# Optimization experiments

Hardware: AMD Instinct MI355X
Metric: run time of the kernel (lower is better)

Reference implementation:

```python
import jax, jax.numpy as jnp
import numpy as np

UP = 512      # up_size
RADIUS = 60   # revise crop radius -> 120x120 squares
COEF = 1.5    # COM threshold coefficient
DOT = 4       # intensity-adjust circle radius
B = 16
M = 4
BASE = 128


def _affine_grid(theta, H, W):
    # torch F.affine_grid, align_corners=False. theta: (2,3) -> grid (H,W,2) with (x,y)
    xs = (2.0 * jnp.arange(W, dtype=jnp.float32) + 1.0) / W - 1.0
    ys = (2.0 * jnp.arange(H, dtype=jnp.float32) + 1.0) / H - 1.0
    X, Y = jnp.meshgrid(xs, ys)  # (H,W), X varies along width
    base = jnp.stack([X, Y, jnp.ones_like(X)], axis=-1)  # (H,W,3)
    return base @ theta.T  # (H,W,2)


def _gs_one(im, gr):
    # torch F.grid_sample, bilinear, zero padding, align_corners=False
    # im: (C,H,W), gr: (Hg,Wg,2) -> (C,Hg,Wg)
    C, H, W = im.shape
    x = ((gr[..., 0] + 1.0) * W - 1.0) * 0.5
    y = ((gr[..., 1] + 1.0) * H - 1.0) * 0.5
    x0 = jnp.floor(x)
    y0 = jnp.floor(y)
    wx = x - x0
    wy = y - y0

    def tap(ix, iy, w):
        valid = (ix >= 0) & (ix < W) & (iy >= 0) & (iy < H)
        ii = jnp.clip(iy, 0, H - 1).astype(jnp.int32)
        jj = jnp.clip(ix, 0, W - 1).astype(jnp.int32)
        return im[:, ii, jj] * (jnp.where(valid, w, 0.0))[None]

    return (tap(x0, y0, (1 - wx) * (1 - wy))
            + tap(x0 + 1, y0, wx * (1 - wy))
            + tap(x0, y0 + 1, (1 - wx) * wy)
            + tap(x0 + 1, y0 + 1, wx * wy))


_grid_sample = jax.vmap(_gs_one)  # (B,C,H,W),(B,Hg,Wg,2)->(B,C,Hg,Wg)


def _inv2x3(theta):
    # append [0,0,1], invert 3x3, keep top 2 rows (as in Joint.forward)
    n = theta.shape[0]
    bottom = jnp.broadcast_to(jnp.array([[0.0, 0.0, 1.0]], jnp.float32), (n, 1, 3))
    full = jnp.concatenate([theta, bottom], axis=1)
    return jnp.linalg.inv(full)[:, :2]


def _com(img, mask, coef):
    # center_of_mass: threshold = coef * mean over mask, intensity-weighted centroid
    H, W = img.shape
    msum = jnp.maximum(mask.sum(), 1.0)
    thr = (img.sum() / msum) * coef
    w = jnp.where(img > thr, img, 0.0)
    tot = w.sum() + 1e-8
    cx = (w.sum(axis=1) * jnp.arange(H, dtype=img.dtype)).sum() / tot  # row
    cy = (w.sum(axis=0) * jnp.arange(W, dtype=img.dtype)).sum() / tot  # col
    return cx, cy


def _revise(image, masks_rot, inv_theta, adj, radius, coef, dot):
    # revise_size_on_affine_gpu with adj_para given and pare_reverse=True
    d = 2 * radius
    yy, xx = jnp.meshgrid(jnp.arange(d), jnp.arange(d), indexing='ij')
    small_sq = ((yy - radius) ** 2 + (xx - radius) ** 2) <= dot ** 2  # dot mask

    def per_item(img_i, new_i, mask_i, th_i, a_i):
        cx, cy = _com(new_i, mask_i, coef)
        x0 = jnp.round(cx).astype(jnp.int32) - radius
        y0 = jnp.round(cy).astype(jnp.int32) - radius
        small = jax.lax.dynamic_slice(img_i[0], (x0, y0), (d, d))
        small = jnp.where(small_sq, small / a_i, small)  # pare_reverse=True -> divide
        out = _gs_one(small[None], _affine_grid(th_i, d, d))  # (1,d,d)
        return jax.lax.dynamic_update_slice(img_i, out, (0, x0, y0))

    img = image
    for j in range(masks_rot.shape[0]):
        mj = masks_rot[j]                 # (B,H,W) float 0/1
        new = image[:, 0] * mj            # COM always from original image*mask
        img = jax.vmap(per_item)(img, new, mj, inv_theta, adj)
    return img


def setup_inputs() -> dict:
    key = jax.random.key(0)
    ks = jax.random.split(key, 6)
    predicted_base = jax.random.uniform(ks[0], (B, 1, BASE, BASE), jnp.float32)
    e = 0.05 * jax.random.normal(ks[1], (B, 4), jnp.float32)
    sc = (jnp.zeros((B, 2, 3), jnp.float32)
          .at[:, 0, 0].set(1.0 + e[:, 0]).at[:, 0, 1].set(e[:, 1])
          .at[:, 1, 0].set(e[:, 2]).at[:, 1, 1].set(1.0 + e[:, 3]))
    ang = jax.random.uniform(ks[2], (B,), jnp.float32, -0.2, 0.2)
    rot = (jnp.zeros((B, 2, 3), jnp.float32)
           .at[:, 0, 0].set(jnp.cos(ang)).at[:, 0, 1].set(-jnp.sin(ang))
           .at[:, 1, 0].set(jnp.sin(ang)).at[:, 1, 1].set(jnp.cos(ang)))
    t = jax.random.uniform(ks[3], (B, 2), jnp.float32, -0.05, 0.05)
    tr = (jnp.zeros((B, 2, 3), jnp.float32)
          .at[:, 0, 0].set(1.0).at[:, 1, 1].set(1.0)
          .at[:, 0, 2].set(t[:, 0]).at[:, 1, 2].set(t[:, 1]))
    adj = jax.random.uniform(ks[4], (B,), jnp.float32, 0.9, 1.1)
    centers = [(128, 128), (128, 384), (384, 128), (384, 384)]
    yy, xx = np.meshgrid(np.arange(UP), np.arange(UP), indexing='ij')
    masks = np.stack([((yy - cy) ** 2 + (xx - cx) ** 2 <= 30 ** 2).astype(np.float32)
                      for (cy, cx) in centers])
    return dict(predicted_base=predicted_base, scaler_shear=sc, rotation=rot,
                translation=tr, adj_mask=adj, masks=jnp.asarray(masks))


def reference(predicted_base, scaler_shear, rotation, translation, adj_mask, masks):
    b = predicted_base.shape[0]
    it1 = _inv2x3(scaler_shear)
    it2 = _inv2x3(rotation)
    it3 = _inv2x3(translation)
    base_inp = jax.image.resize(predicted_base, (b, 1, UP, UP), method='linear')
    mk_grid = jax.vmap(lambda th: _affine_grid(th, UP, UP))
    g1, g2, g3 = mk_grid(it1), mk_grid(it2), mk_grid(it3)
    pred_trans = _grid_sample(base_inp, g3)
    pred_rot = _grid_sample(pred_trans, g2)
    pred_input = _grid_sample(pred_rot, g1)
    # rotate masks through grid_2 then grid_1, threshold at 0.5
    new_masks = []
    for j in range(masks.shape[0]):
        bm = jnp.broadcast_to(masks[j][None, None], (b, 1, UP, UP))
        rm = _grid_sample(_grid_sample(bm, g2), g1)
        new_masks.append(rm[:, 0] >= 0.5)
    masks_rot = jnp.stack(new_masks)  # (M,B,UP,UP) bool
    pred_revise = _revise(pred_input, masks_rot.astype(pred_input.dtype), it1,
                          adj_mask, RADIUS, COEF, DOT)
    return (base_inp, pred_input, pred_revise, masks_rot)
```

## Files before the change

### kernel.cpp

```cpp
#include <hip/hip_runtime.h>
#include <math.h>
#include <limits.h>

#define NPIX (512*512)
#define NB 16
#define RAD 60
#define DSZ 120
#define PSTR 121
#define GTS 48
#define GSTR 49


__device__ __forceinline__ float gs_bilinear(const float* img, int H, int W,
                                             float gx, float gy) {
    float x = ((gx + 1.0f) * (float)W - 1.0f) * 0.5f;
    float y = ((gy + 1.0f) * (float)H - 1.0f) * 0.5f;
    float xf = floorf(x), yf = floorf(y);
    int ix = (int)xf, iy = (int)yf;
    float wx = x - xf, wy = y - yf;
    float v = 0.0f;
    bool vx0 = (ix >= 0) && (ix < W);
    bool vx1 = (ix >= -1) && (ix < W - 1);
    bool vy0 = (iy >= 0) && (iy < H);
    bool vy1 = (iy >= -1) && (iy < H - 1);
    if (vx0 && vy0) v += img[iy*W + ix]         * ((1.0f - wx) * (1.0f - wy));
    if (vx1 && vy0) v += img[iy*W + ix + 1]     * (wx * (1.0f - wy));
    if (vx0 && vy1) v += img[(iy+1)*W + ix]     * ((1.0f - wx) * wy);
    if (vx1 && vy1) v += img[(iy+1)*W + ix + 1] * (wx * wy);
    return v;
}

__device__ __forceinline__ float gs_bilinear_patch(const float* img, float gx, float gy) {
    float x = ((gx + 1.0f) * 120.0f - 1.0f) * 0.5f;
    float y = ((gy + 1.0f) * 120.0f - 1.0f) * 0.5f;
    float xf = floorf(x), yf = floorf(y);
    int ix = (int)xf, iy = (int)yf;
    float wx = x - xf, wy = y - yf;
    float v = 0.0f;
    bool vx0 = (ix >= 0) && (ix < 120);
    bool vx1 = (ix >= -1) && (ix < 119);
    bool vy0 = (iy >= 0) && (iy < 120);
    bool vy1 = (iy >= -1) && (iy < 119);
    if (vx0 && vy0) v += img[iy*PSTR + ix]         * ((1.0f - wx) * (1.0f - wy));
    if (vx1 && vy0) v += img[iy*PSTR + ix + 1]     * (wx * (1.0f - wy));
    if (vx0 && vy1) v += img[(iy+1)*PSTR + ix]     * ((1.0f - wx) * wy);
    if (vx1 && vy1) v += img[(iy+1)*PSTR + ix + 1] * (wx * wy);
    return v;
}

__global__ void __launch_bounds__(256) k_init(const float* __restrict__ base,
                                              const float* __restrict__ sc,
                                              const float* __restrict__ rot,
                                              const float* __restrict__ tr,
                                              const float* __restrict__ masks,
                                              float* __restrict__ out0,
                                              float* __restrict__ ws_inv,
                                              int* __restrict__ bbox,
                                              unsigned* __restrict__ occ,
                                              int* __restrict__ qcount) {
    int bid = blockIdx.x;
    if (bid < 4096) {
        int b = bid >> 8;
        int p4 = (bid & 255) * 256 + threadIdx.x;
        int p = p4 * 4;
        int y = p >> 9, x0p = p & 511;
        const float* src = base + b * 128 * 128;
        float r[4];
        float sy = (float)y * 0.25f - 0.375f;
        float fy0 = floorf(sy);
        int iy = (int)fy0;
        float fy = sy - fy0;
        int iy0 = min(max(iy, 0), 127), iy1 = min(max(iy + 1, 0), 127);
        #pragma unroll
        for (int k = 0; k < 4; ++k) {
            int x = x0p + k;
            float sx = (float)x * 0.25f - 0.375f;
            float fx0 = floorf(sx);
            int ix = (int)fx0;
            float fx = sx - fx0;
            int ix0 = min(max(ix, 0), 127), ix1 = min(max(ix + 1, 0), 127);
            float v00 = src[iy0 * 128 + ix0], v10 = src[iy0 * 128 + ix1];
            float v01 = src[iy1 * 128 + ix0], v11 = src[iy1 * 128 + ix1];
            r[k] = (v00 * (1.0f - fx) + v10 * fx) * (1.0f - fy)
                 + (v01 * (1.0f - fx) + v11 * fx) * fy;
        }
        *(float4*)(out0 + (size_t)b * NPIX + p) = make_float4(r[0], r[1], r[2], r[3]);
    } else if (bid < 4128) {
        int word = (bid - 4096) * 4 + (threadIdx.x >> 6);
        int lane = threadIdx.x & 63;
        int j = word >> 5, ty = word & 31;
        const float* mk = masks + (size_t)j * NPIX + ty * 16 * 512 + lane * 8;
        int any = 0;
        for (int rr = 0; rr < 16; ++rr) {
            const float4* p = (const float4*)(mk + rr * 512);
            float4 a = p[0], c = p[1];
            if (a.x != 0.f || a.y != 0.f || a.z != 0.f || a.w != 0.f ||
                c.x != 0.f || c.y != 0.f || c.z != 0.f || c.w != 0.f) any = 1;
        }
        unsigned long long bb = __ballot(any);
        if (lane == 0) {
            unsigned wrd = 0;
            for (int tx = 0; tx < 32; ++tx)
                if (bb & (3ull << (2 * tx))) wrd |= 1u << tx;
            occ[j * 32 + ty] = wrd;
        }
    } else {
        int t = threadIdx.x;
        if (t < 48) {
            int m = t >> 4, b = t & 15;
            const float* th = (m == 0 ? sc : (m == 1 ? rot : tr)) + b * 6;
            float a  = th[0], bbv = th[1], tx = th[2];
            float c  = th[3], d   = th[4], ty = th[5];
            float L10 = c / a;
            float dp  = d  - L10 * bbv;
            float typ = ty - L10 * tx;
            float i10 = (0.0f - L10) / dp;
            float i00 = (1.0f - bbv * i10) / a;
            float i11 = 1.0f / dp;
            float i01 = (0.0f - bbv * i11) / a;
            float i12 = (0.0f - typ) / dp;
            float i02 = (0.0f - bbv * i12 - tx) / a;
            float* o = ws_inv + m * 96 + b * 6;
            o[0] = i00; o[1] = i01; o[2] = i02;
            o[3] = i10; o[4] = i11; o[5] = i12;
        }
        bbox[t] = ((t & 3) < 2) ? INT_MAX : INT_MIN;
        if (t == 0) *qcount = 0;
    }
}

__device__ __forceinline__ void gsample_tile(const float* __restrict__ src,
                                             float* __restrict__ dst,
                                             float* __restrict__ dst2,
                                             const float* __restrict__ thetas,
                                             int b, int tile, float* tb) {
    int ox = (tile & 15) * 32, oy = (tile >> 4) * 32;
    const float* th = thetas + b * 6;
    float t0 = th[0], t1 = th[1], t2 = th[2], t3 = th[3], t4 = th[4], t5 = th[5];
    const float* im = src + (size_t)b * NPIX;

    float sxmin = 1e30f, sxmax = -1e30f, symin = 1e30f, symax = -1e30f;
    #pragma unroll
    for (int cy = 0; cy < 2; ++cy)
        #pragma unroll
        for (int cx = 0; cx < 2; ++cx) {
            float X = (2.0f * (float)(ox + cx * 31) + 1.0f) / 512.0f - 1.0f;
            float Y = (2.0f * (float)(oy + cy * 31) + 1.0f) / 512.0f - 1.0f;
            float gx = t0 * X + t1 * Y + t2;
            float gy = t3 * X + t4 * Y + t5;
            float sx = ((gx + 1.0f) * 512.0f - 1.0f) * 0.5f;
            float sy = ((gy + 1.0f) * 512.0f - 1.0f) * 0.5f;
            sxmin = fminf(sxmin, sx); sxmax = fmaxf(sxmax, sx);
            symin = fminf(symin, sy); symax = fmaxf(symax, sy);
        }
    int rx0 = (int)floorf(sxmin) - 1;
    int ry0 = (int)floorf(symin) - 1;
    bool fits = ((int)floorf(sxmax) + 2 - rx0 < GTS) &&
                ((int)floorf(symax) + 2 - ry0 < GTS);

    int t = threadIdx.x;
    int py = oy + (t >> 3);
    int px0 = ox + (t & 7) * 4;
    float Y = (2.0f * (float)py + 1.0f) / 512.0f - 1.0f;
    float r[4];

    if (fits) {
        for (int i = t; i < GTS * GTS; i += 256) {
            int rr = i / GTS, cc = i - rr * GTS;
            int gy_ = ry0 + rr, gx_ = rx0 + cc;
            float v = 0.0f;
            if (gx_ >= 0 && gx_ < 512 && gy_ >= 0 && gy_ < 512)
                v = im[gy_ * 512 + gx_];
            tb[rr * GSTR + cc] = v;
        }
        __syncthreads();
        #pragma unroll
        for (int k = 0; k < 4; ++k) {
            float X = (2.0f * (float)(px0 + k) + 1.0f) / 512.0f - 1.0f;
            float gx = t0 * X + t1 * Y + t2;
            float gy = t3 * X + t4 * Y + t5;
            float x = ((gx + 1.0f) * 512.0f - 1.0f) * 0.5f;
            float y = ((gy + 1.0f) * 512.0f - 1.0f) * 0.5f;
            float xf = floorf(x), yf = floorf(y);
            int ix = (int)xf, iy = (int)yf;
            float wx = x - xf, wy = y - yf;
            int lx = ix - rx0, ly = iy - ry0;
            float v;
            v  = tb[ly * GSTR + lx]           * ((1.0f - wx) * (1.0f - wy));
            v += tb[ly * GSTR + lx + 1]       * (wx * (1.0f - wy));
            v += tb[(ly + 1) * GSTR + lx]     * ((1.0f - wx) * wy);
            v += tb[(ly + 1) * GSTR + lx + 1] * (wx * wy);
            r[k] = v;
        }
    } else {
        #pragma unroll
        for (int k = 0; k < 4; ++k) {
            float X = (2.0f * (float)(px0 + k) + 1.0f) / 512.0f - 1.0f;
            float gx = t0 * X + t1 * Y + t2;
            float gy = t3 * X + t4 * Y + t5;
            r[k] = gs_bilinear(im, 512, 512, gx, gy);
        }
    }
    float4 v4 = make_float4(r[0], r[1], r[2], r[3]);
    size_t op = (size_t)b * NPIX + py * 512 + px0;
    *(float4*)(dst + op) = v4;
    if (dst2) *(float4*)(dst2 + op) = v4;
}

__global__ void __launch_bounds__(256) k_g3ot(const float* __restrict__ src,
                                              float* __restrict__ dst,
                                              const float* __restrict__ inv3,
                                              const unsigned* __restrict__ occ,
                                              const float* __restrict__ inv1,
                                              const float* __restrict__ inv2,
                                              unsigned char* __restrict__ otile,
                                              int* __restrict__ queue,
                                              int* __restrict__ qcount) {
    __shared__ float tb[GTS * GSTR];
    int bid = blockIdx.x;
    if (bid < 4096) {
        gsample_tile(src, dst, nullptr, inv3, bid >> 8, bid & 255, tb);
        return;
    }
    int idx = (bid - 4096) * 256 + threadIdx.x;
    int jb = idx >> 10, tile = idx & 1023;
    int j = jb >> 4, b = jb & 15;
    int ty = tile >> 5, tx = tile & 31;
    const float* t1 = inv1 + b * 6;
    const float* t2 = inv2 + b * 6;
    float xs[2] = { (float)(tx * 16), (float)(tx * 16 + 15) };
    float ys[2] = { (float)(ty * 16), (float)(ty * 16 + 15) };
    float sxmin = 1e30f, sxmax = -1e30f, symin = 1e30f, symax = -1e30f;
    for (int cy = 0; cy < 2; ++cy)
        for (int cx = 0; cx < 2; ++cx) {
            float X = (2.0f * xs[cx] + 1.0f) / 512.0f - 1.0f;
            float Y = (2.0f * ys[cy] + 1.0f) / 512.0f - 1.0f;
            float gx = t1[0] * X + t1[1] * Y + t1[2];
            float gy = t1[3] * X + t1[4] * Y + t1[5];
            float sx = ((gx + 1.0f) * 512.0f - 1.0f) * 0.5f;
            float sy = ((gy + 1.0f) * 512.0f - 1.0f) * 0.5f;
            sxmin = fminf(sxmin, sx); sxmax = fmaxf(sxmax, sx);
            symin = fminf(symin, sy); symax = fmaxf(symax, sy);
        }
    int c0 = max((int)floorf(sxmin) - 1, 0), c1 = min((int)floorf(sxmax) + 2, 511);
    int r0 = max((int)floorf(symin) - 1, 0), r1 = min((int)floorf(symax) + 2, 511);
    bool any = false;
    if (c0 <= c1 && r0 <= r1) {
        float A0 = t2[0], A1 = t2[1], A3 = t2[3], A4 = t2[4];
        float Kx = 0.5f * (-511.0f * (A0 + A1) + 512.0f * t2[2] + 511.0f);
        float Ky = 0.5f * (-511.0f * (A3 + A4) + 512.0f * t2[5] + 511.0f);
        float pxmin = A0 * (A0 >= 0.f ? c0 : c1) + A1 * (A1 >= 0.f ? r0 : r1) + Kx;
        float pxmax = A0 * (A0 >= 0.f ? c1 : c0) + A1 * (A1 >= 0.f ? r1 : r0) + Kx;
        float pymin = A3 * (A3 >= 0.f ? c0 : c1) + A4 * (A4 >= 0.f ? r0 : r1) + Ky;
        float pymax = A3 * (A3 >= 0.f ? c1 : c0) + A4 * (A4 >= 0.f ? r1 : r0) + Ky;
        int xlo = max((int)floorf(pxmin) - 1, 0), xhi = min((int)floorf(pxmax) + 2, 511);
        int ylo = max((int)floorf(pymin) - 1, 0), yhi = min((int)floorf(pymax) + 2, 511);
        if (xlo <= xhi && ylo <= yhi)
            for (int tr = ylo >> 4; tr <= yhi >> 4; ++tr)
                for (int tc = xlo >> 4; tc <= xhi >> 4; ++tc)
                    if ((occ[j * 32 + tr] >> tc) & 1u) any = true;
    }
    otile[idx] = any ? 1 : 0;
    if (any) {
        int pos = atomicAdd(qcount, 1);
        queue[pos] = (jb << 10) | tile;
    }
}

__global__ void __launch_bounds__(256) k_gsample(const float* __restrict__ src,
                                                 float* __restrict__ dst,
                                                 float* __restrict__ dst2,
                                                 const float* __restrict__ thetas) {
    __shared__ float tb[GTS * GSTR];
    gsample_tile(src, dst, dst2, thetas, blockIdx.x >> 8, blockIdx.x & 255, tb);
}

__device__ __forceinline__ float rm2_val(const float* mk, const float* t2, int cx_, int ry_) {
    float X2 = (2.0f * (float)cx_ + 1.0f) / 512.0f - 1.0f;
    float Y2 = (2.0f * (float)ry_ + 1.0f) / 512.0f - 1.0f;
    float g2x = t2[0] * X2 + t2[1] * Y2 + t2[2];
    float g2y = t2[3] * X2 + t2[4] * Y2 + t2[5];
    return gs_bilinear(mk, 512, 512, g2x, g2y);
}

__global__ void __launch_bounds__(256) k_zml(const float* __restrict__ masks,
                                             float* __restrict__ out3,
                                             const float* __restrict__ inv1,
                                             const float* __restrict__ inv2,
                                             const unsigned char* __restrict__ otile,
                                             const int* __restrict__ queue,
                                             const int* __restrict__ qcount,
                                             int* __restrict__ bbox) {
    int bid = blockIdx.x;
    if (bid < 2048) {
        const float4 z4 = make_float4(0.f, 0.f, 0.f, 0.f);
        float4* p = (float4*)out3;
        int stride = 2048 * 256;
        for (int i = bid * 256 + threadIdx.x; i < 64 * NPIX / 4; i += stride) {
            int jb = i >> 16;
            int w = i & 65535;
            int y = w >> 7;
            int x = (w << 2) & 511;
            int tile = ((y >> 4) << 5) | (x >> 4);
            if (!otile[(jb << 10) | tile]) p[i] = z4;
        }
        return;
    }
    __shared__ int sbb[4];
    int n = *qcount;
    for (int q = bid - 2048; q < n; q += 1024) {
        int e = queue[q];
        int jb = e >> 10, tile = e & 1023;
        if (threadIdx.x == 0) { sbb[0] = INT_MAX; sbb[1] = INT_MAX; sbb[2] = INT_MIN; sbb[3] = INT_MIN; }
        __syncthreads();

        int ty = tile >> 5, tx = tile & 31;
        int y = ty * 16 + (threadIdx.x >> 4);
        int x = tx * 16 + (threadIdx.x & 15);
        int j = jb >> 4, b = jb & 15;
        const float* t1 = inv1 + b * 6;
        const float* t2 = inv2 + b * 6;
        const float* mk = masks + (size_t)j * NPIX;

        float X = (2.0f * (float)x + 1.0f) / 512.0f - 1.0f;
        float Y = (2.0f * (float)y + 1.0f) / 512.0f - 1.0f;
        float gx = t1[0] * X + t1[1] * Y + t1[2];
        float gy = t1[3] * X + t1[4] * Y + t1[5];
        float sx = ((gx + 1.0f) * 512.0f - 1.0f) * 0.5f;
        float sy = ((gy + 1.0f) * 512.0f - 1.0f) * 0.5f;
        float xf = floorf(sx), yf = floorf(sy);
        int ix = (int)xf, iy = (int)yf;
        float wx = sx - xf, wy = sy - yf;

        float v = 0.0f;
        bool vx0 = (ix >= 0) && (ix < 512);
        bool vx1 = (ix >= -1) && (ix < 511);
        bool vy0 = (iy >= 0) && (iy < 512);
        bool vy1 = (iy >= -1) && (iy < 511);
        if (vx0 && vy0) v += rm2_val(mk, t2, ix,     iy    ) * ((1.0f - wx) * (1.0f - wy));
        if (vx1 && vy0) v += rm2_val(mk, t2, ix + 1, iy    ) * (wx * (1.0f - wy));
        if (vx0 && vy1) v += rm2_val(mk, t2, ix,     iy + 1) * ((1.0f - wx) * wy);
        if (vx1 && vy1) v += rm2_val(mk, t2, ix + 1, iy + 1) * (wx * wy);

        float res = 0.0f;
        if (v >= 0.5f) {
            res = 1.0f;
            atomicMin(&sbb[0], y); atomicMin(&sbb[1], x);
            atomicMax(&sbb[2], y); atomicMax(&sbb[3], x);
        }
        out3[(size_t)jb * NPIX + y * 512 + x] = res;

        __syncthreads();
        if (threadIdx.x == 0 && sbb[2] != INT_MIN) {
            atomicMin(&bbox[jb * 4 + 0], sbb[0]);
            atomicMin(&bbox[jb * 4 + 1], sbb[1]);
            atomicMax(&bbox[jb * 4 + 2], sbb[2]);
            atomicMax(&bbox[jb * 4 + 3], sbb[3]);
        }
        __syncthreads();
    }
}

__global__ void __launch_bounds__(256) k_stats(const float* __restrict__ pred,
                                               const float* __restrict__ mrot,
                                               const int* __restrict__ bbox,
                                               int* __restrict__ xy) {
    int jb = blockIdx.x;
    int b = jb & 15;
    int rmin = bbox[jb*4+0], cmin = bbox[jb*4+1], rmax = bbox[jb*4+2], cmax = bbox[jb*4+3];
    const float* img = pred + (size_t)b * NPIX;
    const float* mk  = mrot + (size_t)jb * NPIX;
    int lane = threadIdx.x & 63, w = threadIdx.x >> 6;
    int W = cmax - cmin + 1;
    int total = (rmax >= rmin) ? W * (rmax - rmin + 1) : 0;

    double msum = 0.0, isum = 0.0;
    for (int i = threadIdx.x; i < total; i += 256) {
        int r = rmin + i / W, c = cmin + i % W;
        float m = mk[r * 512 + c];
        if (m != 0.0f) {
            msum += (double)m;
            isum += (double)(img[r * 512 + c] * m);
        }
    }
    for (int o = 32; o > 0; o >>= 1) {
        msum += __shfl_down(msum, o, 64);
        isum += __shfl_down(isum, o, 64);
    }
    __shared__ double s0[4], s1[4], s2[4];
    __shared__ double sthr;
    if (lane == 0) { s0[w] = msum; s1[w] = isum; }
    __syncthreads();
    if (threadIdx.x == 0) {
        double M = s0[0] + s0[1] + s0[2] + s0[3];
        double I = s1[0] + s1[1] + s1[2] + s1[3];
        sthr = (I / fmax(M, 1.0)) * 1.5;
    }
    __syncthreads();
    double t = sthr;

    double wsum = 0.0, sy = 0.0, sx = 0.0;
    for (int i = threadIdx.x; i < total; i += 256) {
        int r = rmin + i / W, c = cmin + i % W;
        float m = mk[r * 512 + c];
        if (m != 0.0f) {
            float v = img[r * 512 + c] * m;
            if ((double)v > t) {
                double vd = (double)v;
                wsum += vd;
                sy += vd * (double)r;
                sx += vd * (double)c;
            }
        }
    }
    for (int o = 32; o > 0; o >>= 1) {
        wsum += __shfl_down(wsum, o, 64);
        sy   += __shfl_down(sy,   o, 64);
        sx   += __shfl_down(sx,   o, 64);
    }
    __syncthreads();
    if (lane == 0) { s0[w] = wsum; s1[w] = sy; s2[w] = sx; }
    __syncthreads();
    if (threadIdx.x == 0) {
        double W_ = s0[0] + s0[1] + s0[2] + s0[3];
        double SY = s1[0] + s1[1] + s1[2] + s1[3];
        double SX = s2[0] + s2[1] + s2[2] + s2[3];
        double tot = W_ + 1e-8;
        int x0 = (int)rint(SY / tot) - RAD;
        int y0 = (int)rint(SX / tot) - RAD;
        x0 = min(max(x0, 0), 512 - DSZ);
        y0 = min(max(y0, 0), 512 - DSZ);
        xy[jb * 2 + 0] = x0;
        xy[jb * 2 + 1] = y0;
    }
}

__device__ __forceinline__ void patch_one(float* __restrict__ im, float* __restrict__ patch,
                                          int x0, int y0, float a,
                                          float t0, float t1, float t2,
                                          float t3, float t4, float t5) {
    for (int t = threadIdx.x; t < DSZ * DSZ; t += 1024) {
        int u = t / DSZ, v = t % DSZ;
        float val = im[(x0 + u) * 512 + (y0 + v)];
        int du = u - RAD, dv = v - RAD;
        if (du * du + dv * dv <= 16) val = val / a;
        patch[u * PSTR + v] = val;
    }
    __syncthreads();
    for (int t = threadIdx.x; t < DSZ * DSZ; t += 1024) {
        int py = t / DSZ, px = t % DSZ;
        float X = (2.0f * (float)px + 1.0f) / 120.0f - 1.0f;
        float Y = (2.0f * (float)py + 1.0f) / 120.0f - 1.0f;
        float gx = t0 * X + t1 * Y + t2;
        float gy = t3 * X + t4 * Y + t5;
        float o = gs_bilinear_patch(patch, gx, gy);
        im[(x0 + py) * 512 + (y0 + px)] = o;
    }
}

__global__ void __launch_bounds__(1024) k_patch(float* __restrict__ img,
                                                const int* __restrict__ xy,
                                                const float* __restrict__ inv1,
                                                const float* __restrict__ adj) {
    __shared__ float patch[DSZ * PSTR];
    int b = blockIdx.x >> 2, j = blockIdx.x & 3;
    int rx[4], ry[4];
    #pragma unroll
    for (int k = 0; k < 4; ++k) {
        rx[k] = xy[(k * 16 + b) * 2 + 0];
        ry[k] = xy[(k * 16 + b) * 2 + 1];
    }
    bool overlap = false;
    #pragma unroll
    for (int i = 0; i < 4; ++i)
        #pragma unroll
        for (int k = 0; k < 4; ++k)
            if (i < k && abs(rx[i] - rx[k]) < DSZ && abs(ry[i] - ry[k]) < DSZ)
                overlap = true;

    float a = adj[b];
    float* im = img + (size_t)b * NPIX;
    const float* th = inv1 + b * 6;
    float t0 = th[0], t1 = th[1], t2 = th[2], t3 = th[3], t4 = th[4], t5 = th[5];

    if (!overlap) {
        patch_one(im, patch, rx[j], ry[j], a, t0, t1, t2, t3, t4, t5);
    } else {
        if (j != 0) return;
        for (int jj = 0; jj < 4; ++jj) {
            patch_one(im, patch, rx[jj], ry[jj], a, t0, t1, t2, t3, t4, t5);
            __threadfence_block();
            __syncthreads();
        }
    }
}


extern "C" void kernel_launch(void* const* d_in, const int* in_sizes, int n_in,
                              void* d_out, int out_size, void* d_ws, size_t ws_size,
                              hipStream_t stream) {
    const float* base  = (const float*)d_in[0];
    const float* sc    = (const float*)d_in[1];
    const float* rot   = (const float*)d_in[2];
    const float* tr    = (const float*)d_in[3];
    const float* adj   = (const float*)d_in[4];
    const float* masks = (const float*)d_in[5];

    float* out  = (float*)d_out;
    float* out0 = out;
    float* out1 = out0 + (size_t)NB * NPIX;
    float* out2 = out1 + (size_t)NB * NPIX;
    float* out3 = out2 + (size_t)NB * NPIX;

    float*         inv1   = (float*)d_ws;
    float*         inv2   = inv1 + 96;
    float*         inv3   = inv1 + 192;
    int*           xy     = (int*)((char*)d_ws + 4096);
    int*           bbox   = (int*)((char*)d_ws + 8192);
    unsigned*      occ    = (unsigned*)((char*)d_ws + 12288);
    int*           qcount = (int*)((char*)d_ws + 16128);
    unsigned char* otile  = (unsigned char*)((char*)d_ws + 16384);
    int*           queue  = (int*)((char*)d_ws + 81920);

    k_init<<<4129, 256, 0, stream>>>(base, sc, rot, tr, masks, out0,
                                     (float*)d_ws, bbox, occ, qcount);
    k_g3ot<<<4352, 256, 0, stream>>>(out0, out2, inv3, occ, inv1, inv2,
                                     otile, queue, qcount);
    k_gsample<<<4096, 256, 0, stream>>>(out2, out3, nullptr, inv2);
    k_gsample<<<4096, 256, 0, stream>>>(out3, out1, out2, inv1);
    k_zml<<<3072, 256, 0, stream>>>(masks, out3, inv1, inv2, otile, queue, qcount, bbox);
    k_stats<<<64, 256, 0, stream>>>(out1, out3, bbox, xy);
    k_patch<<<64, 1024, 0, stream>>>(out2, xy, inv1, adj);
}
```

Measured before the change: 248.6 us.

## Fuse upsample and three chained grid samples into one tiled kernel

Replaces the upsample pass and the three separate grid-sample kernels with one kernel. Per output tile it works back through the inverse affine chain to find the source regions, recomputes the upsampled base into shared memory, and applies the translate, rotate and scale samples stage by stage in LDS. This drops the full-resolution intermediate writes and reads between stages and two kernel launches. In exchange each block uses more shared memory and redundantly recomputes halo regions, and tiles whose footprint does not fit fall back to a very expensive nested per-pixel evaluation.

Result: no change. 248.4 us (-0.1%).

```diff
diff --git a/kernel.cpp b/kernel.cpp
--- a/kernel.cpp
+++ b/kernel.cpp
@@ -7,8 +7,13 @@
 #define RAD 60
 #define DSZ 120
 #define PSTR 121
-#define GTS 48
-#define GSTR 49
+
+#define C1 48
+#define SR_S 49
+#define C2 62
+#define ST_S 63
+#define C3 66
+#define SB_S 67
 
 
 __device__ __forceinline__ float gs_bilinear(const float* img, int H, int W,
@@ -48,45 +53,91 @@
     return v;
 }
 
-__global__ void __launch_bounds__(256) k_init(const float* __restrict__ base,
-                                              const float* __restrict__ sc,
-                                              const float* __restrict__ rot,
-                                              const float* __restrict__ tr,
-                                              const float* __restrict__ masks,
-                                              float* __restrict__ out0,
-                                              float* __restrict__ ws_inv,
-                                              int* __restrict__ bbox,
-                                              unsigned* __restrict__ occ,
-                                              int* __restrict__ qcount) {
+__device__ __forceinline__ float upsample_val(const float* __restrict__ src, int y, int x) {
+    float sy = (float)y * 0.25f - 0.375f;
+    float fy0 = floorf(sy);
+    int iy = (int)fy0;
+    float fy = sy - fy0;
+    int iy0 = min(max(iy, 0), 127), iy1 = min(max(iy + 1, 0), 127);
+    float sx = (float)x * 0.25f - 0.375f;
+    float fx0 = floorf(sx);
+    int ix = (int)fx0;
+    float fx = sx - fx0;
+    int ix0 = min(max(ix, 0), 127), ix1 = min(max(ix + 1, 0), 127);
+    float v00 = src[iy0 * 128 + ix0], v10 = src[iy0 * 128 + ix1];
+    float v01 = src[iy1 * 128 + ix0], v11 = src[iy1 * 128 + ix1];
+    return (v00 * (1.0f - fx) + v10 * fx) * (1.0f - fy)
+         + (v01 * (1.0f - fx) + v11 * fx) * fy;
+}
+
+__device__ __forceinline__ void smap512(const float* th, float x, float y,
+                                        float& sx, float& sy) {
+    float X = (2.0f * x + 1.0f) / 512.0f - 1.0f;
+    float Y = (2.0f * y + 1.0f) / 512.0f - 1.0f;
+    float gx = th[0] * X + th[1] * Y + th[2];
+    float gy = th[3] * X + th[4] * Y + th[5];
+    sx = ((gx + 1.0f) * 512.0f - 1.0f) * 0.5f;
+    sy = ((gy + 1.0f) * 512.0f - 1.0f) * 0.5f;
+}
+
+__device__ __forceinline__ void corner_bbox(const float* th, float x0, float x1,
+                                            float y0, float y1,
+                                            int& lx, int& ly, int& w, int& h) {
+    float sxmin = 1e30f, sxmax = -1e30f, symin = 1e30f, symax = -1e30f;
+    #pragma unroll
+    for (int cy = 0; cy < 2; ++cy)
+        #pragma unroll
+        for (int cx = 0; cx < 2; ++cx) {
+            float sx, sy;
+            smap512(th, cx ? x1 : x0, cy ? y1 : y0, sx, sy);
+            sxmin = fminf(sxmin, sx); sxmax = fmaxf(sxmax, sx);
+            symin = fminf(symin, sy); symax = fmaxf(symax, sy);
+        }
+    lx = (int)floorf(sxmin) - 1;
+    ly = (int)floorf(symin) - 1;
+    w  = (int)floorf(sxmax) + 2 - lx + 1;
+    h  = (int)floorf(symax) + 2 - ly + 1;
+}
+
+__device__ __forceinline__ float fb_binp(const float* bs, int x, int y) {
+    if (x < 0 || x >= 512 || y < 0 || y >= 512) return 0.0f;
+    return upsample_val(bs, y, x);
+}
+__device__ __forceinline__ float fb_trans(const float* bs, const float* th3, int x, int y) {
+    if (x < 0 || x >= 512 || y < 0 || y >= 512) return 0.0f;
+    float sx, sy; smap512(th3, (float)x, (float)y, sx, sy);
+    float xf = floorf(sx), yf = floorf(sy);
+    int ix = (int)xf, iy = (int)yf;
+    float wx = sx - xf, wy = sy - yf;
+    return fb_binp(bs, ix, iy)         * ((1.0f - wx) * (1.0f - wy))
+         + fb_binp(bs, ix + 1, iy)     * (wx * (1.0f - wy))
+         + fb_binp(bs, ix, iy + 1)     * ((1.0f - wx) * wy)
+         + fb_binp(bs, ix + 1, iy + 1) * (wx * wy);
+}
+__device__ __forceinline__ float fb_rot(const float* bs, const float* th2,
+                                        const float* th3, int x, int y) {
+    if (x < 0 || x >= 512 || y < 0 || y >= 512) return 0.0f;
+    float sx, sy; smap512(th2, (float)x, (float)y, sx, sy);
+    float xf = floorf(sx), yf = floorf(sy);
+    int ix = (int)xf, iy = (int)yf;
+    float wx = sx - xf, wy = sy - yf;
+    return fb_trans(bs, th3, ix, iy)         * ((1.0f - wx) * (1.0f - wy))
+         + fb_trans(bs, th3, ix + 1, iy)     * (wx * (1.0f - wy))
+         + fb_trans(bs, th3, ix, iy + 1)     * ((1.0f - wx) * wy)
+         + fb_trans(bs, th3, ix + 1, iy + 1) * (wx * wy);
+}
+
+__global__ void __launch_bounds__(256) k_pre(const float* __restrict__ sc,
+                                             const float* __restrict__ rot,
+                                             const float* __restrict__ tr,
+                                             const float* __restrict__ masks,
+                                             float* __restrict__ ws_inv,
+                                             int* __restrict__ bbox,
+                                             unsigned* __restrict__ occ,
+                                             int* __restrict__ qcount) {
     int bid = blockIdx.x;
-    if (bid < 4096) {
-        int b = bid >> 8;
-        int p4 = (bid & 255) * 256 + threadIdx.x;
-        int p = p4 * 4;
-        int y = p >> 9, x0p = p & 511;
-        const float* src = base + b * 128 * 128;
-        float r[4];
-        float sy = (float)y * 0.25f - 0.375f;
-        float fy0 = floorf(sy);
-        int iy = (int)fy0;
-        float fy = sy - fy0;
-        int iy0 = min(max(iy, 0), 127), iy1 = min(max(iy + 1, 0), 127);
-        #pragma unroll
-        for (int k = 0; k < 4; ++k) {
-            int x = x0p + k;
-            float sx = (float)x * 0.25f - 0.375f;
-            float fx0 = floorf(sx);
-            int ix = (int)fx0;
-            float fx = sx - fx0;
-            int ix0 = min(max(ix, 0), 127), ix1 = min(max(ix + 1, 0), 127);
-            float v00 = src[iy0 * 128 + ix0], v10 = src[iy0 * 128 + ix1];
-            float v01 = src[iy1 * 128 + ix0], v11 = src[iy1 * 128 + ix1];
-            r[k] = (v00 * (1.0f - fx) + v10 * fx) * (1.0f - fy)
-                 + (v01 * (1.0f - fx) + v11 * fx) * fy;
-        }
-        *(float4*)(out0 + (size_t)b * NPIX + p) = make_float4(r[0], r[1], r[2], r[3]);
-    } else if (bid < 4128) {
-        int word = (bid - 4096) * 4 + (threadIdx.x >> 6);
+    if (bid < 32) {
+        int word = bid * 4 + (threadIdx.x >> 6);
         int lane = threadIdx.x & 63;
         int j = word >> 5, ty = word & 31;
         const float* mk = masks + (size_t)j * NPIX + ty * 16 * 512 + lane * 8;
@@ -129,150 +180,174 @@
     }
 }
 
-__device__ __forceinline__ void gsample_tile(const float* __restrict__ src,
-                                             float* __restrict__ dst,
-                                             float* __restrict__ dst2,
-                                             const float* __restrict__ thetas,
-                                             int b, int tile, float* tb) {
+__global__ void __launch_bounds__(256) k_main(const float* __restrict__ base,
+                                              float* __restrict__ out0,
+                                              float* __restrict__ out1,
+                                              float* __restrict__ out2,
+                                              const float* __restrict__ inv1,
+                                              const float* __restrict__ inv2,
+                                              const float* __restrict__ inv3,
+                                              const unsigned* __restrict__ occ,
+                                              unsigned char* __restrict__ otile,
+                                              int* __restrict__ queue,
+                                              int* __restrict__ qcount) {
+    __shared__ float sb[C3 * SB_S];
+    __shared__ float st[C2 * ST_S];
+    __shared__ float sr[C1 * SR_S];
+    int bid = blockIdx.x;
+
+    if (bid >= 4096) {
+        int idx = (bid - 4096) * 256 + threadIdx.x;
+        int jb = idx >> 10, tile = idx & 1023;
+        int j = jb >> 4, bb_ = jb & 15;
+        int ty = tile >> 5, tx = tile & 31;
+        const float* t1 = inv1 + bb_ * 6;
+        const float* t2 = inv2 + bb_ * 6;
+        float xs[2] = { (float)(tx * 16), (float)(tx * 16 + 15) };
+        float ys[2] = { (float)(ty * 16), (float)(ty * 16 + 15) };
+        float sxmin = 1e30f, sxmax = -1e30f, symin = 1e30f, symax = -1e30f;
+        for (int cy = 0; cy < 2; ++cy)
+            for (int cx = 0; cx < 2; ++cx) {
+                float sx, sy;
+                smap512(t1, xs[cx], ys[cy], sx, sy);
+                sxmin = fminf(sxmin, sx); sxmax = fmaxf(sxmax, sx);
+                symin = fminf(symin, sy); symax = fmaxf(symax, sy);
+            }
+        int c0 = max((int)floorf(sxmin) - 1, 0), c1 = min((int)floorf(sxmax) + 2, 511);
+        int r0 = max((int)floorf(symin) - 1, 0), r1 = min((int)floorf(symax) + 2, 511);
+        bool any = false;
+        if (c0 <= c1 && r0 <= r1) {
+            float A0 = t2[0], A1 = t2[1], A3 = t2[3], A4 = t2[4];
+            float Kx = 0.5f * (-511.0f * (A0 + A1) + 512.0f * t2[2] + 511.0f);
+            float Ky = 0.5f * (-511.0f * (A3 + A4) + 512.0f * t2[5] + 511.0f);
+            float pxmin = A0 * (A0 >= 0.f ? c0 : c1) + A1 * (A1 >= 0.f ? r0 : r1) + Kx;
+            float pxmax = A0 * (A0 >= 0.f ? c1 : c0) + A1 * (A1 >= 0.f ? r1 : r0) + Kx;
+            float pymin = A3 * (A3 >= 0.f ? c0 : c1) + A4 * (A4 >= 0.f ? r0 : r1) + Ky;
+            float pymax = A3 * (A3 >= 0.f ? c1 : c0) + A4 * (A4 >= 0.f ? r1 : r0) + Ky;
+            int xlo = max((int)floorf(pxmin) - 1, 0), xhi = min((int)floorf(pxmax) + 2, 511);
+            int ylo = max((int)floorf(pymin) - 1, 0), yhi = min((int)floorf(pymax) + 2, 511);
+            if (xlo <= xhi && ylo <= yhi)
+                for (int tr_ = ylo >> 4; tr_ <= yhi >> 4; ++tr_)
+                    for (int tc = xlo >> 4; tc <= xhi >> 4; ++tc)
+                        if ((occ[j * 32 + tr_] >> tc) & 1u) any = true;
+        }
+        otile[idx] = any ? 1 : 0;
+        if (any) {
+            int pos = atomicAdd(qcount, 1);
+            queue[pos] = (jb << 10) | tile;
+        }
+        return;
+    }
+
+    int b = bid >> 8, tile = bid & 255;
     int ox = (tile & 15) * 32, oy = (tile >> 4) * 32;
-    const float* th = thetas + b * 6;
-    float t0 = th[0], t1 = th[1], t2 = th[2], t3 = th[3], t4 = th[4], t5 = th[5];
-    const float* im = src + (size_t)b * NPIX;
-
-    float sxmin = 1e30f, sxmax = -1e30f, symin = 1e30f, symax = -1e30f;
+    const float* bsrc = base + b * 128 * 128;
+    float a1[6], a2[6], a3[6];
     #pragma unroll
-    for (int cy = 0; cy < 2; ++cy)
-        #pragma unroll
-        for (int cx = 0; cx < 2; ++cx) {
-            float X = (2.0f * (float)(ox + cx * 31) + 1.0f) / 512.0f - 1.0f;
-            float Y = (2.0f * (float)(oy + cy * 31) + 1.0f) / 512.0f - 1.0f;
-            float gx = t0 * X + t1 * Y + t2;
-            float gy = t3 * X + t4 * Y + t5;
-            float sx = ((gx + 1.0f) * 512.0f - 1.0f) * 0.5f;
-            float sy = ((gy + 1.0f) * 512.0f - 1.0f) * 0.5f;
-            sxmin = fminf(sxmin, sx); sxmax = fmaxf(sxmax, sx);
-            symin = fminf(symin, sy); symax = fmaxf(symax, sy);
-        }
-    int rx0 = (int)floorf(sxmin) - 1;
-    int ry0 = (int)floorf(symin) - 1;
-    bool fits = ((int)floorf(sxmax) + 2 - rx0 < GTS) &&
-                ((int)floorf(symax) + 2 - ry0 < GTS);
-
+    for (int k = 0; k < 6; ++k) {
+        a1[k] = inv1[b * 6 + k];
+        a2[k] = inv2[b * 6 + k];
+        a3[k] = inv3[b * 6 + k];
+    }
     int t = threadIdx.x;
     int py = oy + (t >> 3);
     int px0 = ox + (t & 7) * 4;
-    float Y = (2.0f * (float)py + 1.0f) / 512.0f - 1.0f;
+
+    {
+        float4 v4 = make_float4(upsample_val(bsrc, py, px0),
+                                upsample_val(bsrc, py, px0 + 1),
+                                upsample_val(bsrc, py, px0 + 2),
+                                upsample_val(bsrc, py, px0 + 3));
+        *(float4*)(out0 + (size_t)b * NPIX + py * 512 + px0) = v4;
+    }
+
+    int lx1, ly1, w1, h1;
+    corner_bbox(a1, (float)ox, (float)(ox + 31), (float)oy, (float)(oy + 31),
+                lx1, ly1, w1, h1);
+    int lx2, ly2, w2, h2;
+    corner_bbox(a2, (float)lx1, (float)(lx1 + w1 - 1), (float)ly1, (float)(ly1 + h1 - 1),
+                lx2, ly2, w2, h2);
+    int lx3, ly3, w3, h3;
+    corner_bbox(a3, (float)lx2, (float)(lx2 + w2 - 1), (float)ly2, (float)(ly2 + h2 - 1),
+                lx3, ly3, w3, h3);
+    bool fits = (w1 <= C1) && (h1 <= C1) && (w2 <= C2) && (h2 <= C2) &&
+                (w3 <= C3) && (h3 <= C3);
+
     float r[4];
-
     if (fits) {
-        for (int i = t; i < GTS * GTS; i += 256) {
-            int rr = i / GTS, cc = i - rr * GTS;
-            int gy_ = ry0 + rr, gx_ = rx0 + cc;
+        for (int i = t; i < w3 * h3; i += 256) {
+            int rr = i / w3, cc = i - rr * w3;
+            int gy = ly3 + rr, gx = lx3 + cc;
             float v = 0.0f;
-            if (gx_ >= 0 && gx_ < 512 && gy_ >= 0 && gy_ < 512)
-                v = im[gy_ * 512 + gx_];
-            tb[rr * GSTR + cc] = v;
+            if (gx >= 0 && gx < 512 && gy >= 0 && gy < 512)
+                v = upsample_val(bsrc, gy, gx);
+            sb[rr * SB_S + cc] = v;
+        }
+        __syncthreads();
+        for (int i = t; i < w2 * h2; i += 256) {
+            int rr = i / w2, cc = i - rr * w2;
+            int gy = ly2 + rr, gx = lx2 + cc;
+            float v = 0.0f;
+            if (gx >= 0 && gx < 512 && gy >= 0 && gy < 512) {
+                float sx, sy; smap512(a3, (float)gx, (float)gy, sx, sy);
+                float xf = floorf(sx), yf = floorf(sy);
+                int ix = (int)xf - lx3, iy = (int)yf - ly3;
+                float wx = sx - xf, wy = sy - yf;
+                v  = sb[iy * SB_S + ix]           * ((1.0f - wx) * (1.0f - wy));
+                v += sb[iy * SB_S + ix + 1]       * (wx * (1.0f - wy));
+                v += sb[(iy + 1) * SB_S + ix]     * ((1.0f - wx) * wy);
+                v += sb[(iy + 1) * SB_S + ix + 1] * (wx * wy);
+            }
+            st[rr * ST_S + cc] = v;
+        }
+        __syncthreads();
+        for (int i = t; i < w1 * h1; i += 256) {
+            int rr = i / w1, cc = i - rr * w1;
+            int gy = ly1 + rr, gx = lx1 + cc;
+            float v = 0.0f;
+            if (gx >= 0 && gx < 512 && gy >= 0 && gy < 512) {
+                float sx, sy; smap512(a2, (float)gx, (float)gy, sx, sy);
+                float xf = floorf(sx), yf = floorf(sy);
+                int ix = (int)xf - lx2, iy = (int)yf - ly2;
+                float wx = sx - xf, wy = sy - yf;
+                v  = st[iy * ST_S + ix]           * ((1.0f - wx) * (1.0f - wy));
+                v += st[iy * ST_S + ix + 1]       * (wx * (1.0f - wy));
+                v += st[(iy + 1) * ST_S + ix]     * ((1.0f - wx) * wy);
+                v += st[(iy + 1) * ST_S + ix + 1] * (wx * wy);
+            }
+            sr[rr * SR_S + cc] = v;
         }
         __syncthreads();
         #pragma unroll
         for (int k = 0; k < 4; ++k) {
-            float X = (2.0f * (float)(px0 + k) + 1.0f) / 512.0f - 1.0f;
-            float gx = t0 * X + t1 * Y + t2;
-            float gy = t3 * X + t4 * Y + t5;
-            float x = ((gx + 1.0f) * 512.0f - 1.0f) * 0.5f;
-            float y = ((gy + 1.0f) * 512.0f - 1.0f) * 0.5f;
-            float xf = floorf(x), yf = floorf(y);
-            int ix = (int)xf, iy = (int)yf;
-            float wx = x - xf, wy = y - yf;
-            int lx = ix - rx0, ly = iy - ry0;
+            float sx, sy; smap512(a1, (float)(px0 + k), (float)py, sx, sy);
+            float xf = floorf(sx), yf = floorf(sy);
+            int ix = (int)xf - lx1, iy = (int)yf - ly1;
+            float wx = sx - xf, wy = sy - yf;
             float v;
-            v  = tb[ly * GSTR + lx]           * ((1.0f - wx) * (1.0f - wy));
-            v += tb[ly * GSTR + lx + 1]       * (wx * (1.0f - wy));
-            v += tb[(ly + 1) * GSTR + lx]     * ((1.0f - wx) * wy);
-            v += tb[(ly + 1) * GSTR + lx + 1] * (wx * wy);
+            v  = sr[iy * SR_S + ix]           * ((1.0f - wx) * (1.0f - wy));
+            v += sr[iy * SR_S + ix + 1]       * (wx * (1.0f - wy));
+            v += sr[(iy + 1) * SR_S + ix]     * ((1.0f - wx) * wy);
+            v += sr[(iy + 1) * SR_S + ix + 1] * (wx * wy);
             r[k] = v;
         }
     } else {
         #pragma unroll
         for (int k = 0; k < 4; ++k) {
-            float X = (2.0f * (float)(px0 + k) + 1.0f) / 512.0f - 1.0f;
-            float gx = t0 * X + t1 * Y + t2;
-            float gy = t3 * X + t4 * Y + t5;
-            r[k] = gs_bilinear(im, 512, 512, gx, gy);
+            float sx, sy; smap512(a1, (float)(px0 + k), (float)py, sx, sy);
+            float xf = floorf(sx), yf = floorf(sy);
+            int ix = (int)xf, iy = (int)yf;
+            float wx = sx - xf, wy = sy - yf;
+            r[k] = fb_rot(bsrc, a2, a3, ix, iy)         * ((1.0f - wx) * (1.0f - wy))
+                 + fb_rot(bsrc, a2, a3, ix + 1, iy)     * (wx * (1.0f - wy))
+                 + fb_rot(bsrc, a2, a3, ix, iy + 1)     * ((1.0f - wx) * wy)
+                 + fb_rot(bsrc, a2, a3, ix + 1, iy + 1) * (wx * wy);
         }
     }
     float4 v4 = make_float4(r[0], r[1], r[2], r[3]);
     size_t op = (size_t)b * NPIX + py * 512 + px0;
-    *(float4*)(dst + op) = v4;
-    if (dst2) *(float4*)(dst2 + op) = v4;
-}
-
-__global__ void __launch_bounds__(256) k_g3ot(const float* __restrict__ src,
-                                              float* __restrict__ dst,
-                                              const float* __restrict__ inv3,
-                                              const unsigned* __restrict__ occ,
-                                              const float* __restrict__ inv1,
-                                              const float* __restrict__ inv2,
-                                              unsigned char* __restrict__ otile,
-                                              int* __restrict__ queue,
-                                              int* __restrict__ qcount) {
-    __shared__ float tb[GTS * GSTR];
-    int bid = blockIdx.x;
-    if (bid < 4096) {
-        gsample_tile(src, dst, nullptr, inv3, bid >> 8, bid & 255, tb);
-        return;
-    }
-    int idx = (bid - 4096) * 256 + threadIdx.x;
-    int jb = idx >> 10, tile = idx & 1023;
-    int j = jb >> 4, b = jb & 15;
-    int ty = tile >> 5, tx = tile & 31;
-    const float* t1 = inv1 + b * 6;
-    const float* t2 = inv2 + b * 6;
-    float xs[2] = { (float)(tx * 16), (float)(tx * 16 + 15) };
-    float ys[2] = { (float)(ty * 16), (float)(ty * 16 + 15) };
-    float sxmin = 1e30f, sxmax = -1e30f, symin = 1e30f, symax = -1e30f;
-    for (int cy = 0; cy < 2; ++cy)
-        for (int cx = 0; cx < 2; ++cx) {
-            float X = (2.0f * xs[cx] + 1.0f) / 512.0f - 1.0f;
-            float Y = (2.0f * ys[cy] + 1.0f) / 512.0f - 1.0f;
-            float gx = t1[0] * X + t1[1] * Y + t1[2];
-            float gy = t1[3] * X + t1[4] * Y + t1[5];
-            float sx = ((gx + 1.0f) * 512.0f - 1.0f) * 0.5f;
-            float sy = ((gy + 1.0f) * 512.0f - 1.0f) * 0.5f;
-            sxmin = fminf(sxmin, sx); sxmax = fmaxf(sxmax, sx);
-            symin = fminf(symin, sy); symax = fmaxf(symax, sy);
-        }
-    int c0 = max((int)floorf(sxmin) - 1, 0), c1 = min((int)floorf(sxmax) + 2, 511);
-    int r0 = max((int)floorf(symin) - 1, 0), r1 = min((int)floorf(symax) + 2, 511);
-    bool any = false;
-    if (c0 <= c1 && r0 <= r1) {
-        float A0 = t2[0], A1 = t2[1], A3 = t2[3], A4 = t2[4];
-        float Kx = 0.5f * (-511.0f * (A0 + A1) + 512.0f * t2[2] + 511.0f);
-        float Ky = 0.5f * (-511.0f * (A3 + A4) + 512.0f * t2[5] + 511.0f);
-        float pxmin = A0 * (A0 >= 0.f ? c0 : c1) + A1 * (A1 >= 0.f ? r0 : r1) + Kx;
-        float pxmax = A0 * (A0 >= 0.f ? c1 : c0) + A1 * (A1 >= 0.f ? r1 : r0) + Kx;
-        float pymin = A3 * (A3 >= 0.f ? c0 : c1) + A4 * (A4 >= 0.f ? r0 : r1) + Ky;
-        float pymax = A3 * (A3 >= 0.f ? c1 : c0) + A4 * (A4 >= 0.f ? r1 : r0) + Ky;
-        int xlo = max((int)floorf(pxmin) - 1, 0), xhi = min((int)floorf(pxmax) + 2, 511);
-        int ylo = max((int)floorf(pymin) - 1, 0), yhi = min((int)floorf(pymax) + 2, 511);
-        if (xlo <= xhi && ylo <= yhi)
-            for (int tr = ylo >> 4; tr <= yhi >> 4; ++tr)
-                for (int tc = xlo >> 4; tc <= xhi >> 4; ++tc)
-                    if ((occ[j * 32 + tr] >> tc) & 1u) any = true;
-    }
-    otile[idx] = any ? 1 : 0;
-    if (any) {
-        int pos = atomicAdd(qcount, 1);
-        queue[pos] = (jb << 10) | tile;
-    }
-}
-
-__global__ void __launch_bounds__(256) k_gsample(const float* __restrict__ src,
-                                                 float* __restrict__ dst,
-                                                 float* __restrict__ dst2,
-                                                 const float* __restrict__ thetas) {
-    __shared__ float tb[GTS * GSTR];
-    gsample_tile(src, dst, dst2, thetas, blockIdx.x >> 8, blockIdx.x & 255, tb);
+    *(float4*)(out1 + op) = v4;
+    *(float4*)(out2 + op) = v4;
 }
 
 __device__ __forceinline__ float rm2_val(const float* mk, const float* t2, int cx_, int ry_) {
@@ -522,12 +597,9 @@
     unsigned char* otile  = (unsigned char*)((char*)d_ws + 16384);
     int*           queue  = (int*)((char*)d_ws + 81920);
 
-    k_init<<<4129, 256, 0, stream>>>(base, sc, rot, tr, masks, out0,
-                                     (float*)d_ws, bbox, occ, qcount);
-    k_g3ot<<<4352, 256, 0, stream>>>(out0, out2, inv3, occ, inv1, inv2,
-                                     otile, queue, qcount);
-    k_gsample<<<4096, 256, 0, stream>>>(out2, out3, nullptr, inv2);
-    k_gsample<<<4096, 256, 0, stream>>>(out3, out1, out2, inv1);
+    k_pre<<<33, 256, 0, stream>>>(sc, rot, tr, masks, (float*)d_ws, bbox, occ, qcount);
+    k_main<<<4352, 256, 0, stream>>>(base, out0, out1, out2, inv1, inv2, inv3,
+                                     occ, otile, queue, qcount);
     k_zml<<<3072, 256, 0, stream>>>(masks, out3, inv1, inv2, otile, queue, qcount, bbox);
     k_stats<<<64, 256, 0, stream>>>(out1, out3, bbox, xy);
     k_patch<<<64, 1024, 0, stream>>>(out2, xy, inv1, adj);
```
